# Kernel tuning notes

Measured on AMD Instinct MI355X. Metric: run time of the kernel, lower is better.

The kernel has to match this reference:

```python
import jax, jax.numpy as jnp
import numpy as np

EPS = 1e-5

def layer_norm(x, gamma, beta):
    # biased variance (unbiased=False), matching torch code
    mean = jnp.mean(x, axis=-1, keepdims=True)
    var = jnp.mean((x - mean) ** 2, axis=-1, keepdims=True)
    return (x - mean) / jnp.sqrt(var + EPS) * gamma + beta

def setup_inputs() -> dict:
    key = jax.random.key(0)
    ks = jax.random.split(key, 8)
    B, T, C, H = 2, 2048, 768, 12
    Dff = 4 * C
    s = lambda n: 1.0 / np.sqrt(n)
    return {
        "x": jax.random.normal(ks[0], (B, T, C), dtype=jnp.float32),
        "mask": jnp.ones((B, T), dtype=jnp.int32),
        "Wqkv": jax.random.normal(ks[1], (C, 3 * C), dtype=jnp.float32) * s(C),
        "bqkv": jnp.zeros((3 * C,), dtype=jnp.float32),
        "Wp": jax.random.normal(ks[2], (C, C), dtype=jnp.float32) * s(C),
        "bp": jnp.zeros((C,), dtype=jnp.float32),
        "gamma1": jnp.ones((1, 1, C), dtype=jnp.float32),
        "beta1": jnp.zeros((1, 1, C), dtype=jnp.float32),
        "W1": jax.random.normal(ks[3], (C, Dff), dtype=jnp.float32) * s(C),
        "b1": jnp.zeros((Dff,), dtype=jnp.float32),
        "W2": jax.random.normal(ks[4], (Dff, C), dtype=jnp.float32) * s(Dff),
        "b2": jnp.zeros((C,), dtype=jnp.float32),
        "gamma2": jnp.ones((1, 1, C), dtype=jnp.float32),
        "beta2": jnp.zeros((1, 1, C), dtype=jnp.float32),
    }

def reference(x, mask, Wqkv, bqkv, Wp, bp, gamma1, beta1, W1, b1, W2, b2, gamma2, beta2):
    B, T, C = x.shape
    H = 12
    D = C // H
    # --- multi-head attention (hand-rolled QK^T-softmax-V) ---
    qkv = x @ Wqkv + bqkv                                  # (B,T,3C)
    q, k, v = jnp.split(qkv, 3, axis=-1)
    q = q.reshape(B, T, H, D).transpose(0, 2, 1, 3)        # (B,H,T,D)
    k = k.reshape(B, T, H, D).transpose(0, 2, 1, 3)
    v = v.reshape(B, T, H, D).transpose(0, 2, 1, 3)
    scores = jnp.einsum('bhtd,bhsd->bhts', q, k) * (D ** -0.5)  # (B,H,T,T)
    pad = (mask == 0)[:, None, None, :]                    # (B,1,1,T)
    scores = jnp.where(pad, -jnp.inf, scores)
    weights = jax.nn.softmax(scores, axis=-1)
    attn = jnp.einsum('bhts,bhsd->bhtd', weights, v)       # (B,H,T,D)
    attn = attn.transpose(0, 2, 1, 3).reshape(B, T, C)
    attn = attn @ Wp + bp
    # --- post-sublayer LN then residual (as in source) ---
    out = x + layer_norm(attn, gamma1, beta1)
    # --- MLP with exact GELU ---
    h = jax.nn.gelu(out @ W1 + b1, approximate=False)
    mlp = h @ W2 + b2
    out = out + layer_norm(mlp, gamma2, beta2)
    return out
```

## Files before the change

kernel.cpp:

```cpp
#include <hip/hip_runtime.h>
#include <math.h>

#define BB 2
#define TT 2048
#define CC 768
#define NH 12
#define HD 64
#define DFF 3072
#define MM (BB*TT)

typedef _Float16 f16;
typedef unsigned long long u64;
typedef unsigned int u32;
typedef __attribute__((ext_vector_type(8))) _Float16 f16x8;
typedef __attribute__((ext_vector_type(4))) _Float16 f16x4;
typedef __attribute__((ext_vector_type(4))) float f32x4;

#define QSCALE 0.18033688011112042f

#define GLD_LDS(gptr, lptr) \
  __builtin_amdgcn_global_load_lds((const __attribute__((address_space(1))) void*)(gptr), \
                                   (__attribute__((address_space(3))) void*)(lptr), 16, 0, 0)

#if __has_builtin(__builtin_amdgcn_exp2f)
#define EXP2(x) __builtin_amdgcn_exp2f(x)
#else
#define EXP2(x) exp2f(x)
#endif

#if __has_builtin(__builtin_amdgcn_rcpf)
#define RCP(x) __builtin_amdgcn_rcpf(x)
#else
#define RCP(x) (1.f / (x))
#endif

__device__ __forceinline__ float gelu_f(float x)
{
    const float y = fabsf(x) * 0.70710678118654752f;
    const float t = RCP(fmaf(0.3275911f, y, 1.f));
    float p = fmaf(1.061405429f, t, -1.453152027f);
    p = fmaf(p, t, 1.421413741f);
    p = fmaf(p, t, -0.284496736f);
    p = fmaf(p, t, 0.254829592f);
    p = p * t;
    const float e = EXP2(-y * y * 1.4426950408889634f);
    const float er = copysignf(1.f - p * e, x);
    return 0.5f * x * (1.f + er);
}

__global__ __launch_bounds__(256)
void convert_f16(const float* __restrict__ in, f16* __restrict__ out, int n4)
{
    const int i = blockIdx.x * 256 + threadIdx.x;
    if (i >= n4) return;
    float4 v = ((const float4*)in)[i];
    f16x4 o = {(f16)v.x, (f16)v.y, (f16)v.z, (f16)v.w};
    ((f16x4*)out)[i] = o;
}

__global__ __launch_bounds__(256)
void convert_transpose(const float* __restrict__ W, f16* __restrict__ Wt,
                       int K, int N)
{
    __shared__ float tile[32][33];
    const int k0 = blockIdx.x * 32, n0 = blockIdx.y * 32;
    const int r  = threadIdx.x >> 3;
    const int c4 = (threadIdx.x & 7) * 4;
    float4 v = *(const float4*)&W[(size_t)(k0 + r) * N + n0 + c4];
    tile[r][c4 + 0] = v.x; tile[r][c4 + 1] = v.y;
    tile[r][c4 + 2] = v.z; tile[r][c4 + 3] = v.w;
    __syncthreads();
    f16x4 o = {(f16)tile[c4 + 0][r], (f16)tile[c4 + 1][r],
               (f16)tile[c4 + 2][r], (f16)tile[c4 + 3][r]};
    *(f16x4*)&Wt[(size_t)(n0 + r) * K + k0 + c4] = o;
}

template<int TM, int OUT_MODE, int GELU, int SPLITK>
__global__ __launch_bounds__(256)
void gemm_mfma(const f16* __restrict__ A, const f16* __restrict__ Bt,
               const float* __restrict__ bias, void* __restrict__ Cout,
               f16* __restrict__ Vout, const int* __restrict__ maskp,
               int M, int N, int K)
{
    constexpr int NT = (TM == 128) ? 4 : 2;
    constexpr int G  = 512 / TM;
    __shared__ f16 As[2][TM * 32];
    __shared__ f16 Bs[2][128 * 32];

    int id = blockIdx.x;
    int kk = 0;
    if (SPLITK == 2) { kk = id & 1; id >>= 1; }
    const int xcd = id & 7, j = id >> 3;
    const int by = xcd * G + (j & (G - 1));
    const int bx = j / G;
    const int Keff = K / SPLITK;

    const int t = threadIdx.x;
    const int lane = t & 63, w = t >> 6;
    const int fr = lane & 15, quad = lane >> 4;
    const int row0 = by * TM, col0 = bx * 128;
    const int wm = (TM == 128) ? (w & 1) * 64 : 0;
    const int wn = (TM == 128) ? (w >> 1) * 64 : w * 32;

    const int arow = w * (TM / 4) + (lane >> 2);
    const int brow = w * 32 + (lane >> 2);
    const int cg = (((lane & 3) ^ ((lane >> 3) & 3)) * 16);
    const char* ag = (const char*)(A  + (size_t)(row0 + arow) * K + kk * Keff) + cg;
    const char* bg = (const char*)(Bt + (size_t)(col0 + brow) * K + kk * Keff) + cg;
    const size_t rowK = (size_t)K * 2;
    const int wA = w * (TM / 4) * 32;
    const int wB = w * 32 * 32;

    const int sof = (quad ^ ((fr >> 1) & 3)) * 8;

    f32x4 acc[4][NT] = {};

    GLD_LDS(ag, &As[0][wA]);
    if (TM == 128) GLD_LDS(ag + 16 * rowK, &As[0][wA + 16 * 32]);
    GLD_LDS(bg, &Bs[0][wB]);
    GLD_LDS(bg + 16 * rowK, &Bs[0][wB + 16 * 32]);

    for (int k0 = 0; k0 < Keff; k0 += 32) {
        const int buf = (k0 >> 5) & 1;
        __syncthreads();
        if (k0 + 32 < Keff) {
            const size_t kb = (size_t)(k0 + 32) * 2;
            GLD_LDS(ag + kb, &As[buf ^ 1][wA]);
            if (TM == 128) GLD_LDS(ag + kb + 16 * rowK, &As[buf ^ 1][wA + 16 * 32]);
            GLD_LDS(bg + kb, &Bs[buf ^ 1][wB]);
            GLD_LDS(bg + kb + 16 * rowK, &Bs[buf ^ 1][wB + 16 * 32]);
        }
        f16x8 af[4], bf[NT];
#pragma unroll
        for (int mt = 0; mt < 4; ++mt)
            af[mt] = *(const f16x8*)&As[buf][(wm + mt * 16 + fr) * 32 + sof];
#pragma unroll
        for (int nt = 0; nt < NT; ++nt)
            bf[nt] = *(const f16x8*)&Bs[buf][(wn + nt * 16 + fr) * 32 + sof];
#pragma unroll
        for (int mt = 0; mt < 4; ++mt)
#pragma unroll
            for (int nt = 0; nt < NT; ++nt)
                acc[mt][nt] = __builtin_amdgcn_mfma_f32_16x16x32_f16(
                    af[mt], bf[nt], acc[mt][nt], 0, 0, 0);
    }

    float bvs[NT];
#pragma unroll
    for (int nt = 0; nt < NT; ++nt)
        bvs[nt] = (SPLITK == 2 && kk) ? 0.f : bias[col0 + wn + nt * 16 + fr];
    const float qsc = (OUT_MODE == 2 && col0 < CC) ? QSCALE : 1.f;
    f16* outbase = (f16*)Cout + (SPLITK == 2 ? (size_t)kk * M * N : 0);
#pragma unroll
    for (int mt = 0; mt < 4; ++mt) {
        const int rowb = row0 + wm + mt * 16 + quad * 4;
        float mv[4] = {1.f, 1.f, 1.f, 1.f};
        if (OUT_MODE == 2 && col0 >= 1536) {
            int4 mi = *(const int4*)&maskp[rowb];
            mv[0] = mi.x ? 1.f : 0.f; mv[1] = mi.y ? 1.f : 0.f;
            mv[2] = mi.z ? 1.f : 0.f; mv[3] = mi.w ? 1.f : 0.f;
        }
#pragma unroll
        for (int nt = 0; nt < NT; ++nt) {
            const int col = col0 + wn + nt * 16 + fr;
            if (OUT_MODE == 2) {
                if (col0 < 1536) {
#pragma unroll
                    for (int v = 0; v < 4; ++v)
                        ((f16*)Cout)[(size_t)(rowb + v) * 1536 + col]
                            = (f16)((acc[mt][nt][v] + bvs[nt]) * qsc);
                } else {
                    const int dg = col - 1536;
                    const int hh = dg >> 6, dd = dg & 63;
                    const int bq = rowb >> 11, s = rowb & 2047;
                    f16x4 pk = {(f16)((acc[mt][nt][0] + bvs[nt]) * mv[0]),
                                (f16)((acc[mt][nt][1] + bvs[nt]) * mv[1]),
                                (f16)((acc[mt][nt][2] + bvs[nt]) * mv[2]),
                                (f16)((acc[mt][nt][3] + bvs[nt]) * mv[3])};
                    *(f16x4*)&Vout[(size_t)((bq * NH + hh) * HD + dd) * TT + s] = pk;
                }
            } else {
#pragma unroll
                for (int v = 0; v < 4; ++v) {
                    float o = acc[mt][nt][v] + bvs[nt];
                    if (GELU) o = gelu_f(o);
                    outbase[(size_t)(rowb + v) * N + col] = (f16)o;
                }
            }
        }
    }
}

__global__ __launch_bounds__(256)
void attn_mfma(const f16* __restrict__ qkh, const f16* __restrict__ vth,
               const int* __restrict__ mask, f16* __restrict__ out)
{
    __shared__ __align__(16) char smem[50432];
    f16* Qs    = (f16*)smem;
    f16* Mf    = (f16*)smem;
    f16* KsB[2]; KsB[0] = (f16*)(smem + 8192);  KsB[1] = (f16*)(smem + 16384);
    f16* VtB[2]; VtB[0] = (f16*)(smem + 24576); VtB[1] = (f16*)(smem + 32768);
    f16* Ps    = (f16*)(smem + 40960);
    float* lredp = (float*)(smem + 50176);
    float* Ored  = (float*)smem;

    const int id = blockIdx.x;
    const int xcd = id & 7, j = id >> 3;
    const int pair = xcd * 3 + j % 3;
    const int qt = j / 3;
    const int b = pair / NH, h = pair % NH;

    const int t = threadIdx.x, lane = t & 63, w = t >> 6;
    const int wq = w >> 1, ws = w & 1;
    const int fr = lane & 15, quad = lane >> 4;

    const int srow = lane >> 3;
    const int scg  = ((lane & 7) ^ (srow & 7)) * 16;

    const char* qg = (const char*)qkh
        + (size_t)(b * TT + qt * 64 + w * 16 + srow) * 3072 + h * 128 + scg;
    const char* kg = (const char*)qkh
        + (size_t)(b * TT + w * 16 + srow) * 3072 + 1536 + h * 128 + scg;
    const char* vg = (const char*)vth
        + (size_t)((b * NH + h) * HD + w * 16 + srow) * (TT * 2) + scg;

    GLD_LDS(qg,            Qs + (w * 16) * 64);
    GLD_LDS(qg + 8 * 3072, Qs + (w * 16 + 8) * 64);
    GLD_LDS(kg,            KsB[0] + (w * 16) * 64);
    GLD_LDS(kg + 8 * 3072, KsB[0] + (w * 16 + 8) * 64);
    GLD_LDS(vg,            VtB[0] + (w * 16) * 64);
    GLD_LDS(vg + 8 * 4096, VtB[0] + (w * 16 + 8) * 64);
    kg += 64 * 3072;
    vg += 128;

    int4 mi0 = *(const int4*)&mask[b * TT + t * 8];
    int4 mi1 = *(const int4*)&mask[b * TT + t * 8 + 4];
    f16x8 mrow;
    mrow[0] = mi0.x ? (f16)1.f : (f16)0.f; mrow[1] = mi0.y ? (f16)1.f : (f16)0.f;
    mrow[2] = mi0.z ? (f16)1.f : (f16)0.f; mrow[3] = mi0.w ? (f16)1.f : (f16)0.f;
    mrow[4] = mi1.x ? (f16)1.f : (f16)0.f; mrow[5] = mi1.y ? (f16)1.f : (f16)0.f;
    mrow[6] = mi1.z ? (f16)1.f : (f16)0.f; mrow[7] = mi1.w ? (f16)1.f : (f16)0.f;

    __syncthreads();

    const int sw0 = ((0 * 4 + quad) ^ (fr & 7)) * 8;
    const int sw1 = ((1 * 4 + quad) ^ (fr & 7)) * 8;

    f16x8 qf[2][2];
#pragma unroll
    for (int nt = 0; nt < 2; ++nt) {
        qf[nt][0] = *(const f16x8*)&Qs[(wq * 32 + nt * 16 + fr) * 64 + sw0];
        qf[nt][1] = *(const f16x8*)&Qs[(wq * 32 + nt * 16 + fr) * 64 + sw1];
    }
    __syncthreads();
    *(f16x8*)&Mf[t * 8] = mrow;

    f32x4 oacc[2][4] = {};
    f32x4 lacc[2] = {};

    for (int it = 0; it < TT / 64; ++it) {
        const int buf = it & 1;
        __syncthreads();
        if (it != TT / 64 - 1) {
            GLD_LDS(kg,            KsB[buf ^ 1] + (w * 16) * 64);
            GLD_LDS(kg + 8 * 3072, KsB[buf ^ 1] + (w * 16 + 8) * 64);
            GLD_LDS(vg,            VtB[buf ^ 1] + (w * 16) * 64);
            GLD_LDS(vg + 8 * 4096, VtB[buf ^ 1] + (w * 16 + 8) * 64);
            kg += 64 * 3072;
            vg += 128;
        }
        const f16* Ks = KsB[buf];
        const f16* Vt = VtB[buf];

        f32x4 sacc[2][2] = {};
#pragma unroll
        for (int mt = 0; mt < 2; ++mt) {
            f16x8 kf0 = *(const f16x8*)&Ks[(ws * 32 + mt * 16 + fr) * 64 + sw0];
            f16x8 kf1 = *(const f16x8*)&Ks[(ws * 32 + mt * 16 + fr) * 64 + sw1];
#pragma unroll
            for (int nt = 0; nt < 2; ++nt) {
                sacc[mt][nt] = __builtin_amdgcn_mfma_f32_16x16x32_f16(
                    kf0, qf[nt][0], sacc[mt][nt], 0, 0, 0);
                sacc[mt][nt] = __builtin_amdgcn_mfma_f32_16x16x32_f16(
                    kf1, qf[nt][1], sacc[mt][nt], 0, 0, 0);
            }
        }

#pragma unroll
        for (int mt = 0; mt < 2; ++mt)
#pragma unroll
            for (int nt = 0; nt < 2; ++nt) {
                f16x4 pk = {(f16)EXP2(sacc[mt][nt][0]), (f16)EXP2(sacc[mt][nt][1]),
                            (f16)EXP2(sacc[mt][nt][2]), (f16)EXP2(sacc[mt][nt][3])};
                *(f16x4*)&Ps[(wq * 32 + nt * 16 + fr) * 72 + ws * 32 + mt * 16 + quad * 4] = pk;
            }

        f16x8 mf = *(const f16x8*)&Mf[it * 64 + ws * 32 + quad * 8];

        f16x8 pf[2];
#pragma unroll
        for (int mt = 0; mt < 2; ++mt)
            pf[mt] = *(const f16x8*)&Ps[(wq * 32 + mt * 16 + fr) * 72 + ws * 32 + quad * 8];
#pragma unroll
        for (int mt = 0; mt < 2; ++mt) {
            lacc[mt] = __builtin_amdgcn_mfma_f32_16x16x32_f16(pf[mt], mf, lacc[mt], 0, 0, 0);
#pragma unroll
            for (int nt = 0; nt < 4; ++nt) {
                f16x8 vf = *(const f16x8*)&Vt[(nt * 16 + fr) * 64 +
                                              (((ws * 4 + quad) ^ (fr & 7)) * 8)];
                oacc[mt][nt] = __builtin_amdgcn_mfma_f32_16x16x32_f16(
                    pf[mt], vf, oacc[mt][nt], 0, 0, 0);
            }
        }
    }

    __syncthreads();
    if (ws == 1) {
#pragma unroll
        for (int mt = 0; mt < 2; ++mt) {
            const int q = wq * 32 + mt * 16 + quad * 4;
#pragma unroll
            for (int nt = 0; nt < 4; ++nt)
#pragma unroll
                for (int v = 0; v < 4; ++v)
                    Ored[(q + v) * 64 + nt * 16 + fr] = oacc[mt][nt][v];
            if (fr == 0)
#pragma unroll
                for (int v = 0; v < 4; ++v) lredp[q + v] = lacc[mt][v];
        }
    }
    __syncthreads();
    if (ws == 0) {
#pragma unroll
        for (int mt = 0; mt < 2; ++mt) {
            const int q0 = wq * 32 + mt * 16 + quad * 4;
            float linv[4];
#pragma unroll
            for (int v = 0; v < 4; ++v)
                linv[v] = 1.f / (lacc[mt][v] + lredp[q0 + v]);
#pragma unroll
            for (int nt = 0; nt < 4; ++nt)
#pragma unroll
                for (int v = 0; v < 4; ++v) {
                    float o = oacc[mt][nt][v] + Ored[(q0 + v) * 64 + nt * 16 + fr];
                    out[(size_t)(b * TT + qt * 64 + q0 + v) * CC + h * HD + nt * 16 + fr]
                        = (f16)(o * linv[v]);
                }
        }
    }
}

template<int WRITE_H>
__global__ __launch_bounds__(256)
void ln_residual(const float* __restrict__ res,
                 const f16* __restrict__ y0, const f16* __restrict__ y1,
                 const float* __restrict__ gamma, const float* __restrict__ beta,
                 float* __restrict__ outp, f16* __restrict__ outh)
{
    const int row = blockIdx.x;
    const int t = threadIdx.x;
    const f16* yr0 = y0 + (size_t)row * CC;
    const f16* yr1 = y1 + (size_t)row * CC;
    const float v0 = (float)yr0[t]       + (float)yr1[t];
    const float v1 = (float)yr0[t + 256] + (float)yr1[t + 256];
    const float v2 = (float)yr0[t + 512] + (float)yr1[t + 512];
    float s  = v0 + v1 + v2;
    float sq = v0 * v0 + v1 * v1 + v2 * v2;
#pragma unroll
    for (int off = 1; off < 64; off <<= 1) {
        s  += __shfl_xor(s, off);
        sq += __shfl_xor(sq, off);
    }
    __shared__ float red[8];
    if ((t & 63) == 0) { red[t >> 6] = s; red[4 + (t >> 6)] = sq; }
    __syncthreads();
    s  = red[0] + red[1] + red[2] + red[3];
    sq = red[4] + red[5] + red[6] + red[7];
    const float mean = s * (1.f / 768.f);
    const float var  = sq * (1.f / 768.f) - mean * mean;
    const float rstd = rsqrtf(var + 1e-5f);
    const float* rr = res + (size_t)row * CC;
    float* orow = outp + (size_t)row * CC;
    const float o0 = rr[t]       + (v0 - mean) * rstd * gamma[t]       + beta[t];
    const float o1 = rr[t + 256] + (v1 - mean) * rstd * gamma[t + 256] + beta[t + 256];
    const float o2 = rr[t + 512] + (v2 - mean) * rstd * gamma[t + 512] + beta[t + 512];
    orow[t] = o0; orow[t + 256] = o1; orow[t + 512] = o2;
    if (WRITE_H) {
        f16* hrow = outh + (size_t)row * CC;
        hrow[t] = (f16)o0; hrow[t + 256] = (f16)o1; hrow[t + 512] = (f16)o2;
    }
}

extern "C" void kernel_launch(void* const* d_in, const int* in_sizes, int n_in,
                              void* d_out, int out_size, void* d_ws, size_t ws_size,
                              hipStream_t stream)
{
    const float* x     = (const float*)d_in[0];
    const int*   mask  = (const int*)  d_in[1];
    const float* Wqkv  = (const float*)d_in[2];
    const float* bqkv  = (const float*)d_in[3];
    const float* Wp    = (const float*)d_in[4];
    const float* bp    = (const float*)d_in[5];
    const float* g1    = (const float*)d_in[6];
    const float* be1   = (const float*)d_in[7];
    const float* W1    = (const float*)d_in[8];
    const float* b1    = (const float*)d_in[9];
    const float* W2    = (const float*)d_in[10];
    const float* b2    = (const float*)d_in[11];
    const float* g2    = (const float*)d_in[12];
    const float* be2   = (const float*)d_in[13];
    float* outp = (float*)d_out;

    char* wsb = (char*)d_ws;
    f16*   qkh    = (f16*)(wsb);
    f16*   vth    = (f16*)(wsb + 12582912);
    f16*   attnh  = (f16*)(wsb + 18874368);
    f16*   hbuf   = (f16*)(wsb);
    f16*   xh     = (f16*)(wsb + 25165824);
    float* out1f  = (float*)(wsb + 25165824);
    f16*   Wqkvt  = (f16*)(wsb + 31457280);
    f16*   Wpt    = (f16*)(wsb + 34996224);
    f16*   W1t    = (f16*)(wsb + 37748736);
    f16*   W2t    = (f16*)(wsb + 42467328);
    f16*   p0     = (f16*)(wsb + 47185920);
    f16*   p1     = (f16*)(wsb + 53477376);
    f16*   out1h  = (f16*)(wsb + 59768832);

    const dim3 blk(256);

    convert_f16<<<dim3(MM * CC / 1024), blk, 0, stream>>>(x, xh, MM * CC / 4);
    convert_transpose<<<dim3(CC / 32, 3 * CC / 32), blk, 0, stream>>>(Wqkv, Wqkvt, CC, 3 * CC);
    convert_transpose<<<dim3(CC / 32, CC / 32), blk, 0, stream>>>(Wp, Wpt, CC, CC);
    convert_transpose<<<dim3(CC / 32, DFF / 32), blk, 0, stream>>>(W1, W1t, CC, DFF);
    convert_transpose<<<dim3(DFF / 32, CC / 32), blk, 0, stream>>>(W2, W2t, DFF, CC);

    gemm_mfma<128, 2, 0, 1><<<dim3((3 * CC / 128) * (MM / 128)), blk, 0, stream>>>(
        xh, Wqkvt, bqkv, qkh, vth, mask, MM, 3 * CC, CC);
    attn_mfma<<<dim3((TT / 64) * NH * BB), blk, 0, stream>>>(qkh, vth, mask, attnh);
    gemm_mfma<64, 1, 0, 2><<<dim3(2 * (CC / 128) * (MM / 64)), blk, 0, stream>>>(
        attnh, Wpt, bp, p0, nullptr, nullptr, MM, CC, CC);
    ln_residual<1><<<dim3(MM), blk, 0, stream>>>(x, p0, p1, g1, be1, out1f, out1h);
    gemm_mfma<128, 1, 1, 1><<<dim3((DFF / 128) * (MM / 128)), blk, 0, stream>>>(
        out1h, W1t, b1, hbuf, nullptr, nullptr, MM, DFF, CC);
    gemm_mfma<64, 1, 0, 2><<<dim3(2 * (CC / 128) * (MM / 64)), blk, 0, stream>>>(
        hbuf, W2t, b2, p0, nullptr, nullptr, MM, CC, DFF);
    ln_residual<0><<<dim3(MM), blk, 0, stream>>>(out1f, p0, p1, g2, be2, outp, nullptr);
}
```

Baseline: 279.2 us.

## Store K/V in MFMA fragment layout and load attention operands directly to registers

The QKV GEMM epilogue now writes Q, K and V to separate buffers. K and V go into a blocked layout that matches the MFMA fragment order, so the attention kernel can load K, V and Q straight from global memory into registers. This removes the LDS double-buffering and the per-iteration barriers, and shrinks shared memory, which should raise occupancy. The LayerNorm-residual kernel is also rewritten to handle 8 rows per block with one row per half-wave, using vectorized loads and no block-level reduction. The risk is that the K scatter stores in the GEMM epilogue are uncoalesced, and attention now relies on L2 or cache reuse instead of LDS staging.

```diff
diff --git a/kernel.cpp b/kernel.cpp
--- a/kernel.cpp
+++ b/kernel.cpp
@@ -79,8 +79,8 @@
 __global__ __launch_bounds__(256)
 void gemm_mfma(const f16* __restrict__ A, const f16* __restrict__ Bt,
                const float* __restrict__ bias, void* __restrict__ Cout,
-               f16* __restrict__ Vout, const int* __restrict__ maskp,
-               int M, int N, int K)
+               f16* __restrict__ Kout, f16* __restrict__ Vout,
+               const int* __restrict__ maskp, int M, int N, int K)
 {
     constexpr int NT = (TM == 128) ? 4 : 2;
     constexpr int G  = 512 / TM;
@@ -110,7 +110,6 @@
     const size_t rowK = (size_t)K * 2;
     const int wA = w * (TM / 4) * 32;
     const int wB = w * 32 * 32;
-
     const int sof = (quad ^ ((fr >> 1) & 3)) * 8;
 
     f32x4 acc[4][NT] = {};
@@ -149,7 +148,6 @@
 #pragma unroll
     for (int nt = 0; nt < NT; ++nt)
         bvs[nt] = (SPLITK == 2 && kk) ? 0.f : bias[col0 + wn + nt * 16 + fr];
-    const float qsc = (OUT_MODE == 2 && col0 < CC) ? QSCALE : 1.f;
     f16* outbase = (f16*)Cout + (SPLITK == 2 ? (size_t)kk * M * N : 0);
 #pragma unroll
     for (int mt = 0; mt < 4; ++mt) {
@@ -164,20 +162,31 @@
         for (int nt = 0; nt < NT; ++nt) {
             const int col = col0 + wn + nt * 16 + fr;
             if (OUT_MODE == 2) {
-                if (col0 < 1536) {
+                const int bq = rowb >> 11, sb = rowb & 2047;
+                if (col0 < 768) {
 #pragma unroll
                     for (int v = 0; v < 4; ++v)
-                        ((f16*)Cout)[(size_t)(rowb + v) * 1536 + col]
-                            = (f16)((acc[mt][nt][v] + bvs[nt]) * qsc);
+                        ((f16*)Cout)[(size_t)(rowb + v) * 768 + col]
+                            = (f16)((acc[mt][nt][v] + bvs[nt]) * QSCALE);
+                } else if (col0 < 1536) {
+                    const int dg = col - 768;
+                    const int hh = dg >> 6, dd = dg & 63;
+                    f16* kb = Kout + (size_t)(bq * NH + hh) * (TT * HD);
+#pragma unroll
+                    for (int v = 0; v < 4; ++v) {
+                        const int s = sb + v;
+                        kb[((s >> 4) * 128 + (dd >> 3) * 16 + (s & 15)) * 8 + (dd & 7)]
+                            = (f16)(acc[mt][nt][v] + bvs[nt]);
+                    }
                 } else {
                     const int dg = col - 1536;
                     const int hh = dg >> 6, dd = dg & 63;
-                    const int bq = rowb >> 11, s = rowb & 2047;
+                    f16* vb = Vout + (size_t)(bq * NH + hh) * (TT * HD);
                     f16x4 pk = {(f16)((acc[mt][nt][0] + bvs[nt]) * mv[0]),
                                 (f16)((acc[mt][nt][1] + bvs[nt]) * mv[1]),
                                 (f16)((acc[mt][nt][2] + bvs[nt]) * mv[2]),
                                 (f16)((acc[mt][nt][3] + bvs[nt]) * mv[3])};
-                    *(f16x4*)&Vout[(size_t)((bq * NH + hh) * HD + dd) * TT + s] = pk;
+                    *(f16x4*)&vb[((sb >> 3) * 64 + dd) * 8 + (sb & 7)] = pk;
                 }
             } else {
 #pragma unroll
@@ -192,17 +201,15 @@
 }
 
 __global__ __launch_bounds__(256)
-void attn_mfma(const f16* __restrict__ qkh, const f16* __restrict__ vth,
-               const int* __restrict__ mask, f16* __restrict__ out)
-{
-    __shared__ __align__(16) char smem[50432];
-    f16* Qs    = (f16*)smem;
-    f16* Mf    = (f16*)smem;
-    f16* KsB[2]; KsB[0] = (f16*)(smem + 8192);  KsB[1] = (f16*)(smem + 16384);
-    f16* VtB[2]; VtB[0] = (f16*)(smem + 24576); VtB[1] = (f16*)(smem + 32768);
-    f16* Ps    = (f16*)(smem + 40960);
-    float* lredp = (float*)(smem + 50176);
+void attn_mfma(const f16* __restrict__ qh, const f16* __restrict__ kth,
+               const f16* __restrict__ vth, const int* __restrict__ mask,
+               f16* __restrict__ out)
+{
+    __shared__ __align__(16) char smem[16640];
+    f16* Mf = (f16*)smem;
+    f16* Ps = (f16*)(smem + 4096);
     float* Ored  = (float*)smem;
+    float* lredp = (float*)(smem + 16384);
 
     const int id = blockIdx.x;
     const int xcd = id & 7, j = id >> 3;
@@ -214,77 +221,66 @@
     const int wq = w >> 1, ws = w & 1;
     const int fr = lane & 15, quad = lane >> 4;
 
-    const int srow = lane >> 3;
-    const int scg  = ((lane & 7) ^ (srow & 7)) * 16;
-
-    const char* qg = (const char*)qkh
-        + (size_t)(b * TT + qt * 64 + w * 16 + srow) * 3072 + h * 128 + scg;
-    const char* kg = (const char*)qkh
-        + (size_t)(b * TT + w * 16 + srow) * 3072 + 1536 + h * 128 + scg;
-    const char* vg = (const char*)vth
-        + (size_t)((b * NH + h) * HD + w * 16 + srow) * (TT * 2) + scg;
-
-    GLD_LDS(qg,            Qs + (w * 16) * 64);
-    GLD_LDS(qg + 8 * 3072, Qs + (w * 16 + 8) * 64);
-    GLD_LDS(kg,            KsB[0] + (w * 16) * 64);
-    GLD_LDS(kg + 8 * 3072, KsB[0] + (w * 16 + 8) * 64);
-    GLD_LDS(vg,            VtB[0] + (w * 16) * 64);
-    GLD_LDS(vg + 8 * 4096, VtB[0] + (w * 16 + 8) * 64);
-    kg += 64 * 3072;
-    vg += 128;
-
-    int4 mi0 = *(const int4*)&mask[b * TT + t * 8];
-    int4 mi1 = *(const int4*)&mask[b * TT + t * 8 + 4];
-    f16x8 mrow;
-    mrow[0] = mi0.x ? (f16)1.f : (f16)0.f; mrow[1] = mi0.y ? (f16)1.f : (f16)0.f;
-    mrow[2] = mi0.z ? (f16)1.f : (f16)0.f; mrow[3] = mi0.w ? (f16)1.f : (f16)0.f;
-    mrow[4] = mi1.x ? (f16)1.f : (f16)0.f; mrow[5] = mi1.y ? (f16)1.f : (f16)0.f;
-    mrow[6] = mi1.z ? (f16)1.f : (f16)0.f; mrow[7] = mi1.w ? (f16)1.f : (f16)0.f;
+    {
+        int4 mi0 = *(const int4*)&mask[b * TT + t * 8];
+        int4 mi1 = *(const int4*)&mask[b * TT + t * 8 + 4];
+        f16x8 mrow;
+        mrow[0] = mi0.x ? (f16)1.f : (f16)0.f; mrow[1] = mi0.y ? (f16)1.f : (f16)0.f;
+        mrow[2] = mi0.z ? (f16)1.f : (f16)0.f; mrow[3] = mi0.w ? (f16)1.f : (f16)0.f;
+        mrow[4] = mi1.x ? (f16)1.f : (f16)0.f; mrow[5] = mi1.y ? (f16)1.f : (f16)0.f;
+        mrow[6] = mi1.z ? (f16)1.f : (f16)0.f; mrow[7] = mi1.w ? (f16)1.f : (f16)0.f;
+        *(f16x8*)&Mf[t * 8] = mrow;
+    }
+
+    f16x8 qf[2][2];
+#pragma unroll
+    for (int nt = 0; nt < 2; ++nt)
+#pragma unroll
+        for (int ks = 0; ks < 2; ++ks)
+            qf[nt][ks] = *(const f16x8*)&qh[(size_t)(b * TT + qt * 64 + wq * 32 + nt * 16 + fr) * CC
+                                            + h * HD + ks * 32 + quad * 8];
 
     __syncthreads();
 
-    const int sw0 = ((0 * 4 + quad) ^ (fr & 7)) * 8;
-    const int sw1 = ((1 * 4 + quad) ^ (fr & 7)) * 8;
-
-    f16x8 qf[2][2];
-#pragma unroll
-    for (int nt = 0; nt < 2; ++nt) {
-        qf[nt][0] = *(const f16x8*)&Qs[(wq * 32 + nt * 16 + fr) * 64 + sw0];
-        qf[nt][1] = *(const f16x8*)&Qs[(wq * 32 + nt * 16 + fr) * 64 + sw1];
-    }
-    __syncthreads();
-    *(f16x8*)&Mf[t * 8] = mrow;
+    const f16* KB = kth + (size_t)(b * NH + h) * (TT * HD);
+    const f16* VB = vth + (size_t)(b * NH + h) * (TT * HD);
+    int ko[2][2], vo[4];
+#pragma unroll
+    for (int mt = 0; mt < 2; ++mt)
+#pragma unroll
+        for (int ks = 0; ks < 2; ++ks)
+            ko[mt][ks] = ((ws * 2 + mt) * 128 + (ks * 4 + quad) * 16 + fr) * 8;
+#pragma unroll
+    for (int nt = 0; nt < 4; ++nt)
+        vo[nt] = ((ws * 4 + quad) * 64 + nt * 16 + fr) * 8;
 
     f32x4 oacc[2][4] = {};
     f32x4 lacc[2] = {};
 
+#pragma unroll 2
     for (int it = 0; it < TT / 64; ++it) {
-        const int buf = it & 1;
-        __syncthreads();
-        if (it != TT / 64 - 1) {
-            GLD_LDS(kg,            KsB[buf ^ 1] + (w * 16) * 64);
-            GLD_LDS(kg + 8 * 3072, KsB[buf ^ 1] + (w * 16 + 8) * 64);
-            GLD_LDS(vg,            VtB[buf ^ 1] + (w * 16) * 64);
-            GLD_LDS(vg + 8 * 4096, VtB[buf ^ 1] + (w * 16 + 8) * 64);
-            kg += 64 * 3072;
-            vg += 128;
-        }
-        const f16* Ks = KsB[buf];
-        const f16* Vt = VtB[buf];
+        const int ib = it * 4096;
+        f16x8 vf[4];
+#pragma unroll
+        for (int nt = 0; nt < 4; ++nt)
+            vf[nt] = *(const f16x8*)(VB + ib + vo[nt]);
+        f16x8 kf[2][2];
+#pragma unroll
+        for (int mt = 0; mt < 2; ++mt)
+#pragma unroll
+            for (int ks = 0; ks < 2; ++ks)
+                kf[mt][ks] = *(const f16x8*)(KB + ib + ko[mt][ks]);
 
         f32x4 sacc[2][2] = {};
 #pragma unroll
-        for (int mt = 0; mt < 2; ++mt) {
-            f16x8 kf0 = *(const f16x8*)&Ks[(ws * 32 + mt * 16 + fr) * 64 + sw0];
-            f16x8 kf1 = *(const f16x8*)&Ks[(ws * 32 + mt * 16 + fr) * 64 + sw1];
+        for (int mt = 0; mt < 2; ++mt)
 #pragma unroll
             for (int nt = 0; nt < 2; ++nt) {
                 sacc[mt][nt] = __builtin_amdgcn_mfma_f32_16x16x32_f16(
-                    kf0, qf[nt][0], sacc[mt][nt], 0, 0, 0);
+                    kf[mt][0], qf[nt][0], sacc[mt][nt], 0, 0, 0);
                 sacc[mt][nt] = __builtin_amdgcn_mfma_f32_16x16x32_f16(
-                    kf1, qf[nt][1], sacc[mt][nt], 0, 0, 0);
+                    kf[mt][1], qf[nt][1], sacc[mt][nt], 0, 0, 0);
             }
-        }
 
 #pragma unroll
         for (int mt = 0; mt < 2; ++mt)
@@ -296,7 +292,6 @@
             }
 
         f16x8 mf = *(const f16x8*)&Mf[it * 64 + ws * 32 + quad * 8];
-
         f16x8 pf[2];
 #pragma unroll
         for (int mt = 0; mt < 2; ++mt)
@@ -305,12 +300,9 @@
         for (int mt = 0; mt < 2; ++mt) {
             lacc[mt] = __builtin_amdgcn_mfma_f32_16x16x32_f16(pf[mt], mf, lacc[mt], 0, 0, 0);
 #pragma unroll
-            for (int nt = 0; nt < 4; ++nt) {
-                f16x8 vf = *(const f16x8*)&Vt[(nt * 16 + fr) * 64 +
-                                              (((ws * 4 + quad) ^ (fr & 7)) * 8)];
+            for (int nt = 0; nt < 4; ++nt)
                 oacc[mt][nt] = __builtin_amdgcn_mfma_f32_16x16x32_f16(
-                    pf[mt], vf, oacc[mt][nt], 0, 0, 0);
-            }
+                    pf[mt], vf[nt], oacc[mt][nt], 0, 0, 0);
         }
     }
 
@@ -357,37 +349,48 @@
                  const float* __restrict__ gamma, const float* __restrict__ beta,
                  float* __restrict__ outp, f16* __restrict__ outh)
 {
-    const int row = blockIdx.x;
     const int t = threadIdx.x;
-    const f16* yr0 = y0 + (size_t)row * CC;
-    const f16* yr1 = y1 + (size_t)row * CC;
-    const float v0 = (float)yr0[t]       + (float)yr1[t];
-    const float v1 = (float)yr0[t + 256] + (float)yr1[t + 256];
-    const float v2 = (float)yr0[t + 512] + (float)yr1[t + 512];
-    float s  = v0 + v1 + v2;
-    float sq = v0 * v0 + v1 * v1 + v2 * v2;
-#pragma unroll
-    for (int off = 1; off < 64; off <<= 1) {
+    const int row = blockIdx.x * 8 + (t >> 5);
+    const int c0 = (t & 31) * 24;
+    const f16* yr0 = y0 + (size_t)row * CC + c0;
+    const f16* yr1 = y1 + (size_t)row * CC + c0;
+    float v[24];
+    float s = 0.f, sq = 0.f;
+#pragma unroll
+    for (int i = 0; i < 3; ++i) {
+        f16x8 a = *(const f16x8*)(yr0 + i * 8);
+        f16x8 bb = *(const f16x8*)(yr1 + i * 8);
+#pragma unroll
+        for (int jj = 0; jj < 8; ++jj) {
+            float vv = (float)a[jj] + (float)bb[jj];
+            v[i * 8 + jj] = vv; s += vv; sq += vv * vv;
+        }
+    }
+#pragma unroll
+    for (int off = 1; off < 32; off <<= 1) {
         s  += __shfl_xor(s, off);
         sq += __shfl_xor(sq, off);
     }
-    __shared__ float red[8];
-    if ((t & 63) == 0) { red[t >> 6] = s; red[4 + (t >> 6)] = sq; }
-    __syncthreads();
-    s  = red[0] + red[1] + red[2] + red[3];
-    sq = red[4] + red[5] + red[6] + red[7];
     const float mean = s * (1.f / 768.f);
     const float var  = sq * (1.f / 768.f) - mean * mean;
     const float rstd = rsqrtf(var + 1e-5f);
-    const float* rr = res + (size_t)row * CC;
-    float* orow = outp + (size_t)row * CC;
-    const float o0 = rr[t]       + (v0 - mean) * rstd * gamma[t]       + beta[t];
-    const float o1 = rr[t + 256] + (v1 - mean) * rstd * gamma[t + 256] + beta[t + 256];
-    const float o2 = rr[t + 512] + (v2 - mean) * rstd * gamma[t + 512] + beta[t + 512];
-    orow[t] = o0; orow[t + 256] = o1; orow[t + 512] = o2;
-    if (WRITE_H) {
-        f16* hrow = outh + (size_t)row * CC;
-        hrow[t] = (f16)o0; hrow[t + 256] = (f16)o1; hrow[t + 512] = (f16)o2;
+    const float* rr = res + (size_t)row * CC + c0;
+    float* orow = outp + (size_t)row * CC + c0;
+#pragma unroll
+    for (int i = 0; i < 6; ++i) {
+        float4 r4 = *(const float4*)(rr + i * 4);
+        float4 g4 = *(const float4*)(gamma + c0 + i * 4);
+        float4 b4 = *(const float4*)(beta + c0 + i * 4);
+        float4 o;
+        o.x = r4.x + (v[i*4+0] - mean) * rstd * g4.x + b4.x;
+        o.y = r4.y + (v[i*4+1] - mean) * rstd * g4.y + b4.y;
+        o.z = r4.z + (v[i*4+2] - mean) * rstd * g4.z + b4.z;
+        o.w = r4.w + (v[i*4+3] - mean) * rstd * g4.w + b4.w;
+        *(float4*)(orow + i * 4) = o;
+        if (WRITE_H) {
+            f16x4 h4 = {(f16)o.x, (f16)o.y, (f16)o.z, (f16)o.w};
+            *(f16x4*)(outh + (size_t)row * CC + c0 + i * 4) = h4;
+        }
     }
 }
 
@@ -412,7 +415,8 @@
     float* outp = (float*)d_out;
 
     char* wsb = (char*)d_ws;
-    f16*   qkh    = (f16*)(wsb);
+    f16*   qhb    = (f16*)(wsb);
+    f16*   kth    = (f16*)(wsb + 6291456);
     f16*   vth    = (f16*)(wsb + 12582912);
     f16*   attnh  = (f16*)(wsb + 18874368);
     f16*   hbuf   = (f16*)(wsb);
@@ -435,14 +439,14 @@
     convert_transpose<<<dim3(DFF / 32, CC / 32), blk, 0, stream>>>(W2, W2t, DFF, CC);
 
     gemm_mfma<128, 2, 0, 1><<<dim3((3 * CC / 128) * (MM / 128)), blk, 0, stream>>>(
-        xh, Wqkvt, bqkv, qkh, vth, mask, MM, 3 * CC, CC);
-    attn_mfma<<<dim3((TT / 64) * NH * BB), blk, 0, stream>>>(qkh, vth, mask, attnh);
+        xh, Wqkvt, bqkv, qhb, kth, vth, mask, MM, 3 * CC, CC);
+    attn_mfma<<<dim3((TT / 64) * NH * BB), blk, 0, stream>>>(qhb, kth, vth, mask, attnh);
     gemm_mfma<64, 1, 0, 2><<<dim3(2 * (CC / 128) * (MM / 64)), blk, 0, stream>>>(
-        attnh, Wpt, bp, p0, nullptr, nullptr, MM, CC, CC);
-    ln_residual<1><<<dim3(MM), blk, 0, stream>>>(x, p0, p1, g1, be1, out1f, out1h);
+        attnh, Wpt, bp, p0, nullptr, nullptr, nullptr, MM, CC, CC);
+    ln_residual<1><<<dim3(MM / 8), blk, 0, stream>>>(x, p0, p1, g1, be1, out1f, out1h);
     gemm_mfma<128, 1, 1, 1><<<dim3((DFF / 128) * (MM / 128)), blk, 0, stream>>>(
-        out1h, W1t, b1, hbuf, nullptr, nullptr, MM, DFF, CC);
+        out1h, W1t, b1, hbuf, nullptr, nullptr, nullptr, MM, DFF, CC);
     gemm_mfma<64, 1, 0, 2><<<dim3(2 * (CC / 128) * (MM / 64)), blk, 0, stream>>>(
-        hbuf, W2t, b2, p0, nullptr, nullptr, MM, CC, DFF);
-    ln_residual<0><<<dim3(MM), blk, 0, stream>>>(out1f, p0, p1, g2, be2, outp, nullptr);
-}
+        hbuf, W2t, b2, p0, nullptr, nullptr, nullptr, MM, CC, DFF);
+    ln_residual<0><<<dim3(MM / 8), blk, 0, stream>>>(out1f, p0, p1, g2, be2, outp, nullptr);
+}
```

Measured after the change: 277.4 us. No clear change (-0.7%).
